# Kernel tuning notes

Measured on AMD Instinct MI355X. Metric: run time of the kernel, lower is better.

Reference implementation:

```python
import jax, jax.numpy as jnp
import numpy as np

N_EMBD = 1024  # C; source scales scores by C**-0.5 (n_embd, not head_size)


def setup_inputs() -> dict:
    key = jax.random.key(0)
    kx, kk, kq, kv = jax.random.split(key, 4)
    B, T, C, H = 8, 2048, N_EMBD, 64
    x = jax.random.normal(kx, (B, T, C), dtype=jnp.float32)
    Wk = jax.random.normal(kk, (C, H), dtype=jnp.float32) * (C ** -0.5)
    Wq = jax.random.normal(kq, (C, H), dtype=jnp.float32) * (C ** -0.5)
    Wv = jax.random.normal(kv, (C, H), dtype=jnp.float32) * (C ** -0.5)
    return {"x": x, "Wk": Wk, "Wq": Wq, "Wv": Wv}


def reference(x, Wk, Wq, Wv):
    B, T, C = x.shape
    k = jnp.einsum('btc,ch->bth', x, Wk)
    q = jnp.einsum('btc,ch->bth', x, Wq)
    v = jnp.einsum('btc,ch->bth', x, Wv)
    # scores scaled by C**-0.5 (faithful to source, which uses n_embd not head_size)
    wei = jnp.einsum('bth,bsh->bts', q, k) * (C ** -0.5)  # [B,T,T]
    causal = jnp.tril(jnp.ones((T, T), dtype=bool))
    wei = jnp.where(causal, wei, -jnp.inf)
    wei = jax.nn.softmax(wei, axis=-1)
    # dropout is identity in eval mode
    out = jnp.einsum('bts,bsh->bth', wei, v)
    return out
```

## Files before the change

### kernel.cpp

```cpp
#include <hip/hip_runtime.h>


#define B_ 8
#define T_ 2048
#define C_ 1024
#define H_ 64
#define BTH (B_ * T_ * H_)

typedef unsigned short u16;
typedef float f32x4 __attribute__((ext_vector_type(4)));
typedef __bf16 bf16x8 __attribute__((ext_vector_type(8)));
#define AS1 __attribute__((address_space(1)))
#define AS3 __attribute__((address_space(3)))

__device__ __forceinline__ u16 f2bf(float f) {
  union { float f; unsigned u; } c; c.f = f;
  unsigned u = c.u;
  return (u16)((u + 0x7FFFu + ((u >> 16) & 1u)) >> 16);
}

__device__ __forceinline__ bf16x8 cvt8(const float4 a, const float4 b) {
  bf16x8 r;
  r[0] = (__bf16)a.x; r[1] = (__bf16)a.y; r[2] = (__bf16)a.z; r[3] = (__bf16)a.w;
  r[4] = (__bf16)b.x; r[5] = (__bf16)b.y; r[6] = (__bf16)b.z; r[7] = (__bf16)b.w;
  return r;
}

__global__ __launch_bounds__(256)
void wpack(const float* __restrict__ Wk, const float* __restrict__ Wq,
           const float* __restrict__ Wv, u16* __restrict__ Wct) {
  const int g  = blockIdx.x;
  const int k0 = blockIdx.y * 64;
  const float* __restrict__ W = (g == 0) ? Wk : (g == 1) ? Wq : Wv;
#pragma unroll
  for (int it = 0; it < 16; ++it) {
    const int idx = it * 256 + threadIdx.x;
    const int kk = k0 + (idx >> 6), h = idx & 63;
    Wct[(size_t)(g * 64 + h) * C_ + kk] = f2bf(W[(size_t)kk * H_ + h]);
  }
}

__global__ __launch_bounds__(256)
void qkv_gemm(const float* __restrict__ x, const u16* __restrict__ Wct,
              u16* __restrict__ ws) {
  __shared__ u16 As[32 * 128];
  const int tid  = threadIdx.x;
  const int wave = tid >> 6, lane = tid & 63;
  const int l15 = lane & 15, quad = lane >> 4;
  const int r0 = blockIdx.x * 32;
  const int srow = tid >> 3, sseg = tid & 7;
  const float* __restrict__ xsrc = x + (size_t)(r0 + srow) * C_ + sseg * 16;
  u16* const wdst0 = As + srow * 128 + ((2 * sseg)     ^ (srow & 15)) * 8;
  u16* const wdst1 = As + srow * 128 + ((2 * sseg + 1) ^ (srow & 15)) * 8;
  const u16* __restrict__ wp = Wct + (size_t)(wave * 48 + l15) * C_ + quad * 8;
  const u16* const ard0 = As + l15 * 128;
  const u16* const ard1 = As + (16 + l15) * 128;
  const f32x4 z = {0.f, 0.f, 0.f, 0.f};
  f32x4 acc[2][3];
#pragma unroll
  for (int m = 0; m < 2; ++m)
#pragma unroll
    for (int ni = 0; ni < 3; ++ni) acc[m][ni] = z;

#pragma unroll 1
  for (int ks = 0; ks < 8; ++ks) {
    const int k0 = ks * 128;
    float4 xa0 = *(const float4*)(xsrc + k0);
    float4 xa1 = *(const float4*)(xsrc + k0 + 4);
    float4 xa2 = *(const float4*)(xsrc + k0 + 8);
    float4 xa3 = *(const float4*)(xsrc + k0 + 12);
    bf16x8 Bf[3][4];
#pragma unroll
    for (int ni = 0; ni < 3; ++ni)
#pragma unroll
      for (int f = 0; f < 4; ++f)
        Bf[ni][f] = *(const bf16x8*)(wp + (size_t)ni * 16 * C_ + k0 + f * 32);
    __syncthreads();
    *(bf16x8*)wdst0 = cvt8(xa0, xa1);
    *(bf16x8*)wdst1 = cvt8(xa2, xa3);
    __syncthreads();
#pragma unroll
    for (int f = 0; f < 4; ++f) {
      const int co = (((4 * f + quad) ^ l15) * 8);
      const bf16x8 a0 = *(const bf16x8*)(ard0 + co);
      const bf16x8 a1 = *(const bf16x8*)(ard1 + co);
#pragma unroll
      for (int ni = 0; ni < 3; ++ni) {
        acc[0][ni] = __builtin_amdgcn_mfma_f32_16x16x32_bf16(a0, Bf[ni][f], acc[0][ni], 0, 0, 0);
        acc[1][ni] = __builtin_amdgcn_mfma_f32_16x16x32_bf16(a1, Bf[ni][f], acc[1][ni], 0, 0, 0);
      }
    }
  }
  const float SCLL = 0.03125f * 1.44269504088896f;
  const int bb = r0 >> 11;
#pragma unroll
  for (int m = 0; m < 2; ++m) {
    const int rowg = r0 + m * 16;
    const int tb = (rowg & 2047) + quad * 4;
#pragma unroll
    for (int ni = 0; ni < 3; ++ni) {
      const int col = wave * 48 + ni * 16 + l15;
      const int g = col >> 6, h = col & 63;
      f32x4 a = acc[m][ni];
      if (g == 1) { a[0] *= SCLL; a[1] *= SCLL; a[2] *= SCLL; a[3] *= SCLL; }
      if (g < 2) {
        u16* op = ws + (size_t)g * BTH + (size_t)(rowg + quad * 4) * H_ + h;
#pragma unroll
        for (int r = 0; r < 4; ++r) op[(size_t)r * H_] = f2bf(a[r]);
      } else {
        uint2 pk;
        pk.x = (unsigned)f2bf(a[0]) | ((unsigned)f2bf(a[1]) << 16);
        pk.y = (unsigned)f2bf(a[2]) | ((unsigned)f2bf(a[3]) << 16);
        *(uint2*)(ws + (size_t)2 * BTH + (size_t)(bb * H_ + h) * T_ + tb) = pk;
      }
    }
  }
}

__global__ __launch_bounds__(128)
void flash(const u16* __restrict__ ws, float* __restrict__ out) {
  __shared__ u16 Ks[2][64 * 64];
  __shared__ u16 Vs[2][64 * 64];
  __shared__ __bf16 Pt[2][16 * 72];
  const u16* __restrict__ kg = ws;
  const u16* __restrict__ qg = ws + BTH;
  const u16* __restrict__ vt = ws + (size_t)2 * BTH;
  const int b    = blockIdx.y;
  const int j    = 63 - (int)blockIdx.x;
  const int tid  = threadIdx.x;
  const int wv   = tid >> 6;
  const int lane = tid & 63;
  const int l15  = lane & 15, quad = lane >> 4;
  const int qt   = 2 * j + wv;
  const int t0   = qt * 16;
  const int ns   = (2 * j + 5) >> 2;
  const u16* kb0 = kg + (size_t)b * T_ * H_;
  const u16* vb0 = vt + (size_t)b * H_ * T_;
  const int srow = tid >> 3, scp = tid & 7;
  const u16* qrow = qg + ((size_t)(b * T_ + t0 + l15)) * H_ + quad * 8;
  const bf16x8 qf0 = *(const bf16x8*)qrow;
  const bf16x8 qf1 = *(const bf16x8*)(qrow + 32);
  __bf16* pt = &Pt[wv][0];
  const f32x4 z = {0.f, 0.f, 0.f, 0.f};
  f32x4 o[4];
  float lr[4] = {0.f, 0.f, 0.f, 0.f};
#pragma unroll
  for (int hi = 0; hi < 4; ++hi) o[hi] = z;

#pragma unroll
  for (int jj = 0; jj < 4; ++jj) {
    const int row = jj * 16 + srow;
    const int sc  = scp ^ (row & 7);
    __builtin_amdgcn_global_load_lds(
        (const AS1 unsigned*)(kb0 + (size_t)row * H_ + sc * 8),
        (AS3 unsigned*)(&Ks[0][(jj * 128 + tid) * 8]), 16, 0, 0);
    __builtin_amdgcn_global_load_lds(
        (const AS1 unsigned*)(vb0 + (size_t)row * T_ + sc * 8),
        (AS3 unsigned*)(&Vs[0][(jj * 128 + tid) * 8]), 16, 0, 0);
  }
  __syncthreads();

#pragma unroll 1
  for (int st = 0; st < ns; ++st) {
    const int cur = st & 1;
    if (st + 1 < ns) {
      const int s1 = (st + 1) * 64;
#pragma unroll
      for (int jj = 0; jj < 4; ++jj) {
        const int row = jj * 16 + srow;
        const int sc  = scp ^ (row & 7);
        __builtin_amdgcn_global_load_lds(
            (const AS1 unsigned*)(kb0 + (size_t)(s1 + row) * H_ + sc * 8),
            (AS3 unsigned*)(&Ks[cur ^ 1][(jj * 128 + tid) * 8]), 16, 0, 0);
        __builtin_amdgcn_global_load_lds(
            (const AS1 unsigned*)(vb0 + (size_t)row * T_ + s1 + sc * 8),
            (AS3 unsigned*)(&Vs[cur ^ 1][(jj * 128 + tid) * 8]), 16, 0, 0);
      }
    }
    const u16* Kc = &Ks[cur][0];
    const u16* Vc = &Vs[cur][0];
    const int sw = (l15 & 7);
    f32x4 s[4];
#pragma unroll
    for (int ni = 0; ni < 4; ++ni) {
      const u16* kr = Kc + (ni * 16 + l15) * 64;
      const bf16x8 k0 = *(const bf16x8*)(kr + ((quad       ^ sw) * 8));
      const bf16x8 k1 = *(const bf16x8*)(kr + (((4 + quad) ^ sw) * 8));
      s[ni] = __builtin_amdgcn_mfma_f32_16x16x32_bf16(qf0, k0, z, 0, 0, 0);
      s[ni] = __builtin_amdgcn_mfma_f32_16x16x32_bf16(qf1, k1, s[ni], 0, 0, 0);
    }
    if (st == ns - 1) {
      const int s0 = st * 64;
#pragma unroll
      for (int ni = 0; ni < 4; ++ni)
#pragma unroll
        for (int r = 0; r < 4; ++r)
          if (s0 + ni * 16 + l15 > t0 + quad * 4 + r) s[ni][r] = -1e30f;
    }
    float p[4][4];
#pragma unroll
    for (int ni = 0; ni < 4; ++ni)
#pragma unroll
      for (int r = 0; r < 4; ++r) p[ni][r] = __builtin_amdgcn_exp2f(s[ni][r]);
#pragma unroll
    for (int r = 0; r < 4; ++r)
      lr[r] += (p[0][r] + p[1][r]) + (p[2][r] + p[3][r]);
#pragma unroll
    for (int ni = 0; ni < 4; ++ni)
#pragma unroll
      for (int r = 0; r < 4; ++r)
        pt[(quad * 4 + r) * 72 + ni * 16 + l15] = (__bf16)p[ni][r];
    asm volatile("s_waitcnt lgkmcnt(0)" ::: "memory");
    const bf16x8 pa0 = *(const bf16x8*)(pt + l15 * 72 + quad * 8);
    const bf16x8 pa1 = *(const bf16x8*)(pt + l15 * 72 + 32 + quad * 8);
    asm volatile("" ::: "memory");
#pragma unroll
    for (int hi = 0; hi < 4; ++hi) {
      const u16* vr = Vc + (hi * 16 + l15) * 64;
      const bf16x8 v0 = *(const bf16x8*)(vr + ((quad       ^ sw) * 8));
      const bf16x8 v1 = *(const bf16x8*)(vr + (((4 + quad) ^ sw) * 8));
      o[hi] = __builtin_amdgcn_mfma_f32_16x16x32_bf16(pa0, v0, o[hi], 0, 0, 0);
      o[hi] = __builtin_amdgcn_mfma_f32_16x16x32_bf16(pa1, v1, o[hi], 0, 0, 0);
    }
    __syncthreads();
  }
#pragma unroll
  for (int d = 1; d < 16; d <<= 1)
#pragma unroll
    for (int r = 0; r < 4; ++r) lr[r] += __shfl_xor(lr[r], d, 64);
  float* ob = out + ((size_t)b * T_ + t0 + quad * 4) * H_ + l15;
#pragma unroll
  for (int r = 0; r < 4; ++r) {
    const float inv = 1.0f / lr[r];
#pragma unroll
    for (int hi = 0; hi < 4; ++hi)
      ob[(size_t)r * H_ + 16 * hi] = o[hi][r] * inv;
  }
}

extern "C" void kernel_launch(void* const* d_in, const int* in_sizes, int n_in,
                              void* d_out, int out_size, void* d_ws, size_t ws_size,
                              hipStream_t stream) {
  const float* x  = (const float*)d_in[0];
  const float* Wk = (const float*)d_in[1];
  const float* Wq = (const float*)d_in[2];
  const float* Wv = (const float*)d_in[3];
  u16*   ws  = (u16*)d_ws;
  u16*   Wct = ws + (size_t)3 * BTH;
  float* out = (float*)d_out;
  wpack<<<dim3(3, 16), 256, 0, stream>>>(Wk, Wq, Wv, Wct);
  qkv_gemm<<<dim3(512), 256, 0, stream>>>(x, Wct, ws);
  flash<<<dim3(64, B_), 128, 0, stream>>>(ws, out);
}
```

Measured before the change: 160.2 us.

## Split causal attention KV range into chunks with partial outputs and reduce kernel

The flash kernel now uses 256-thread blocks that each cover 4 query tiles and at most 4 KV steps. Each long causal row is split into up to 8 chunks, which spreads the work across 144x8 blocks and evens out the triangular imbalance. Partial numerators and row sums go to a workspace buffer. A new reduce kernel sums them and normalises, at the cost of an extra launch and extra global traffic for the partials. The split works without max tracking because the kernel already exponentiates scores with no running max.

After: 142.9 us. 10.8% less time.

```diff
diff --git a/kernel.cpp b/kernel.cpp
--- a/kernel.cpp
+++ b/kernel.cpp
@@ -117,23 +117,29 @@
   }
 }
 
-__global__ __launch_bounds__(128)
-void flash(const u16* __restrict__ ws, float* __restrict__ out) {
+__global__ __launch_bounds__(256)
+void flash(const u16* __restrict__ ws, float* __restrict__ fpart) {
   __shared__ u16 Ks[2][64 * 64];
   __shared__ u16 Vs[2][64 * 64];
-  __shared__ __bf16 Pt[2][16 * 72];
+  __shared__ __bf16 Pt[4][16 * 72];
   const u16* __restrict__ kg = ws;
   const u16* __restrict__ qg = ws + BTH;
   const u16* __restrict__ vt = ws + (size_t)2 * BTH;
-  const int b    = blockIdx.y;
-  const int j    = 63 - (int)blockIdx.x;
+  const int b  = blockIdx.y;
+  const int bx = 143 - (int)blockIdx.x;
+  int c = 0;
+#pragma unroll
+  for (int t = 1; t < 8; ++t)
+    if (34 * t - 2 * t * t <= bx) c = t;
+  const int u = 4 * c + (bx - (34 * c - 2 * c * c));
   const int tid  = threadIdx.x;
   const int wv   = tid >> 6;
   const int lane = tid & 63;
   const int l15  = lane & 15, quad = lane >> 4;
-  const int qt   = 2 * j + wv;
+  const int qt   = 4 * u + wv;
   const int t0   = qt * 16;
-  const int ns   = (2 * j + 5) >> 2;
+  const int st0  = 4 * c;
+  const int stE  = (st0 + 4 < u + 1) ? st0 + 4 : u + 1;
   const u16* kb0 = kg + (size_t)b * T_ * H_;
   const u16* vb0 = vt + (size_t)b * H_ * T_;
   const int srow = tid >> 3, scp = tid & 7;
@@ -147,34 +153,37 @@
 #pragma unroll
   for (int hi = 0; hi < 4; ++hi) o[hi] = z;
 
-#pragma unroll
-  for (int jj = 0; jj < 4; ++jj) {
-    const int row = jj * 16 + srow;
-    const int sc  = scp ^ (row & 7);
-    __builtin_amdgcn_global_load_lds(
-        (const AS1 unsigned*)(kb0 + (size_t)row * H_ + sc * 8),
-        (AS3 unsigned*)(&Ks[0][(jj * 128 + tid) * 8]), 16, 0, 0);
-    __builtin_amdgcn_global_load_lds(
-        (const AS1 unsigned*)(vb0 + (size_t)row * T_ + sc * 8),
-        (AS3 unsigned*)(&Vs[0][(jj * 128 + tid) * 8]), 16, 0, 0);
+  {
+    const int s00 = st0 * 64;
+#pragma unroll
+    for (int jj = 0; jj < 2; ++jj) {
+      const int row = jj * 32 + srow;
+      const int sc  = scp ^ (row & 7);
+      __builtin_amdgcn_global_load_lds(
+          (const AS1 unsigned*)(kb0 + (size_t)(s00 + row) * H_ + sc * 8),
+          (AS3 unsigned*)(&Ks[0][(jj * 256 + tid) * 8]), 16, 0, 0);
+      __builtin_amdgcn_global_load_lds(
+          (const AS1 unsigned*)(vb0 + (size_t)row * T_ + s00 + sc * 8),
+          (AS3 unsigned*)(&Vs[0][(jj * 256 + tid) * 8]), 16, 0, 0);
+    }
   }
   __syncthreads();
 
 #pragma unroll 1
-  for (int st = 0; st < ns; ++st) {
-    const int cur = st & 1;
-    if (st + 1 < ns) {
+  for (int st = st0; st < stE; ++st) {
+    const int cur = (st - st0) & 1;
+    if (st + 1 < stE) {
       const int s1 = (st + 1) * 64;
 #pragma unroll
-      for (int jj = 0; jj < 4; ++jj) {
-        const int row = jj * 16 + srow;
+      for (int jj = 0; jj < 2; ++jj) {
+        const int row = jj * 32 + srow;
         const int sc  = scp ^ (row & 7);
         __builtin_amdgcn_global_load_lds(
             (const AS1 unsigned*)(kb0 + (size_t)(s1 + row) * H_ + sc * 8),
-            (AS3 unsigned*)(&Ks[cur ^ 1][(jj * 128 + tid) * 8]), 16, 0, 0);
+            (AS3 unsigned*)(&Ks[cur ^ 1][(jj * 256 + tid) * 8]), 16, 0, 0);
         __builtin_amdgcn_global_load_lds(
             (const AS1 unsigned*)(vb0 + (size_t)row * T_ + s1 + sc * 8),
-            (AS3 unsigned*)(&Vs[cur ^ 1][(jj * 128 + tid) * 8]), 16, 0, 0);
+            (AS3 unsigned*)(&Vs[cur ^ 1][(jj * 256 + tid) * 8]), 16, 0, 0);
       }
     }
     const u16* Kc = &Ks[cur][0];
@@ -189,7 +198,7 @@
       s[ni] = __builtin_amdgcn_mfma_f32_16x16x32_bf16(qf0, k0, z, 0, 0, 0);
       s[ni] = __builtin_amdgcn_mfma_f32_16x16x32_bf16(qf1, k1, s[ni], 0, 0, 0);
     }
-    if (st == ns - 1) {
+    if (st == u) {
       const int s0 = st * 64;
 #pragma unroll
       for (int ni = 0; ni < 4; ++ni)
@@ -228,14 +237,40 @@
   for (int d = 1; d < 16; d <<= 1)
 #pragma unroll
     for (int r = 0; r < 4; ++r) lr[r] += __shfl_xor(lr[r], d, 64);
-  float* ob = out + ((size_t)b * T_ + t0 + quad * 4) * H_ + l15;
-#pragma unroll
-  for (int r = 0; r < 4; ++r) {
-    const float inv = 1.0f / lr[r];
-#pragma unroll
-    for (int hi = 0; hi < 4; ++hi)
-      ob[(size_t)r * H_ + 16 * hi] = o[hi][r] * inv;
-  }
+  float* po = fpart + (size_t)((b * 128 + qt) * 8 + c) * 1040;
+#pragma unroll
+  for (int hi = 0; hi < 4; ++hi)
+#pragma unroll
+    for (int r = 0; r < 4; ++r)
+      po[(quad * 4 + r) * 64 + hi * 16 + l15] = o[hi][r];
+  if (l15 == 0) {
+#pragma unroll
+    for (int r = 0; r < 4; ++r) po[1024 + quad * 4 + r] = lr[r];
+  }
+}
+
+__global__ __launch_bounds__(256)
+void freduce(const float* __restrict__ fpart, float* __restrict__ out) {
+  const int qt  = blockIdx.x;
+  const int b   = blockIdx.y;
+  const int tid = threadIdx.x;
+  const int nc  = (qt >> 4) + 1;
+  const float* __restrict__ pb = fpart + (size_t)(b * 128 + qt) * 8 * 1040;
+  __shared__ float ls[16];
+  if (tid < 16) {
+    float s = 0.f;
+#pragma unroll 1
+    for (int i = 0; i < nc; ++i) s += pb[(size_t)i * 1040 + 1024 + tid];
+    ls[tid] = s;
+  }
+  __syncthreads();
+  f32x4 a = {0.f, 0.f, 0.f, 0.f};
+#pragma unroll 1
+  for (int i = 0; i < nc; ++i)
+    a += *(const f32x4*)(pb + (size_t)i * 1040 + tid * 4);
+  const float inv = 1.0f / ls[tid >> 4];
+  a[0] *= inv; a[1] *= inv; a[2] *= inv; a[3] *= inv;
+  *(f32x4*)(out + (size_t)(b * T_ + qt * 16 + (tid >> 4)) * H_ + ((tid * 4) & 63)) = a;
 }
 
 extern "C" void kernel_launch(void* const* d_in, const int* in_sizes, int n_in,
@@ -247,8 +282,10 @@
   const float* Wv = (const float*)d_in[3];
   u16*   ws  = (u16*)d_ws;
   u16*   Wct = ws + (size_t)3 * BTH;
+  float* fpart = (float*)(ws + (size_t)3 * BTH + 192 * 1024);
   float* out = (float*)d_out;
   wpack<<<dim3(3, 16), 256, 0, stream>>>(Wk, Wq, Wv, Wct);
   qkv_gemm<<<dim3(512), 256, 0, stream>>>(x, Wct, ws);
-  flash<<<dim3(64, B_), 128, 0, stream>>>(ws, out);
-}
+  flash<<<dim3(144, B_), 256, 0, stream>>>(ws, fpart);
+  freduce<<<dim3(128, B_), 256, 0, stream>>>(fpart, out);
+}
```
